# Kernel optimization log

Hardware: AMD Instinct MI355X
Metric: run time of the kernel (lower is better)

## Reference

```python
import jax, jax.numpy as jnp
import numpy as np

K = 16          # filter order (number of Laplacian powers)
MLP_OUT = 16    # mlp_hid == mlp_out for mlp_nlayers == 1
D_PE = 64       # phi output dim
BN_EPS = 1e-5
B, N, M = 8, 1024, 128
E = 131072


def setup_inputs() -> dict:
    key = jax.random.key(0)
    ks = jax.random.split(key, 12)
    # Symmetric, spectrally-bounded Laplacian surrogate so 15 matrix powers stay finite.
    A = jax.random.normal(ks[0], (B, N, N), dtype=jnp.float32)
    Lap = (A + jnp.swapaxes(A, -1, -2)) * (0.5 / jnp.sqrt(jnp.float32(N)))
    W = jax.random.normal(ks[1], (B, N, M), dtype=jnp.float32)
    edge_index = jax.random.randint(ks[2], (2, E), 0, B * N, dtype=jnp.int64)
    batch = jnp.repeat(jnp.arange(B, dtype=jnp.int64), N)
    # MLP layer (k -> MLP_OUT) + BatchNorm affine params
    lin_w = jax.random.normal(ks[3], (K, MLP_OUT), dtype=jnp.float32) / jnp.sqrt(jnp.float32(K))
    lin_b = jnp.zeros((MLP_OUT,), dtype=jnp.float32)
    bn_gamma = jnp.ones((MLP_OUT,), dtype=jnp.float32)
    bn_beta = jnp.zeros((MLP_OUT,), dtype=jnp.float32)
    # phi: GIN-style 2-layer MLP after neighbor aggregation
    phi_w1 = jax.random.normal(ks[4], (MLP_OUT, D_PE), dtype=jnp.float32) / jnp.sqrt(jnp.float32(MLP_OUT))
    phi_b1 = jnp.zeros((D_PE,), dtype=jnp.float32)
    phi_w2 = jax.random.normal(ks[5], (D_PE, D_PE), dtype=jnp.float32) / jnp.sqrt(jnp.float32(D_PE))
    phi_b2 = jnp.zeros((D_PE,), dtype=jnp.float32)
    return {"Lap": Lap, "W": W, "lin_w": lin_w, "lin_b": lin_b,
            "bn_gamma": bn_gamma, "bn_beta": bn_beta,
            "phi_w1": phi_w1, "phi_b1": phi_b1, "phi_w2": phi_w2, "phi_b2": phi_b2,
            "edge_index": edge_index, "batch": batch}


def _filter(S, W0):
    """Sequential power filter: returns [k, N, M] = [W0, S@W0, S^2@W0, ...]."""
    def step(out, _):
        nxt = S @ out
        return nxt, nxt
    _, rest = jax.lax.scan(step, W0, None, length=K - 1)
    return jnp.concatenate([W0[None], rest], axis=0)


def reference(Lap, W, lin_w, lin_b, bn_gamma, bn_beta,
              phi_w1, phi_b1, phi_w2, phi_b2, edge_index, batch):
    # Batched filter over all graphs: [B, k, N, M] -> [B, N, M, k]
    feat = jax.vmap(_filter)(Lap, W)
    feat = jnp.transpose(feat, (0, 2, 3, 1))
    # Linear over k -> MLP_OUT channels: [B, N, M, C]
    h = feat @ lin_w + lin_b
    # BatchNorm1d (training mode), per-graph statistics over (N, M) per channel,
    # matching the torch per-graph loop where BN sees [M, C, N].
    mean = jnp.mean(h, axis=(1, 2), keepdims=True)
    var = jnp.var(h, axis=(1, 2), keepdims=True)
    h = (h - mean) * jax.lax.rsqrt(var + BN_EPS) * bn_gamma + bn_beta
    h = jax.nn.relu(h)
    # phi: pool random-sample dim M, flatten graphs -> [N_sum, C]
    x = jnp.mean(h, axis=2).reshape(-1, h.shape[-1])
    src, dst = edge_index[0], edge_index[1]
    agg = jax.ops.segment_sum(x[src], dst, num_segments=x.shape[0])
    g = x + agg  # GIN aggregation
    out = jax.nn.relu(g @ phi_w1 + phi_b1) @ phi_w2 + phi_b2  # [N_sum, D_PE]
    return out
```

## Files before the change

### kernel.cpp

```cpp
#include <hip/hip_runtime.h>

#define B 8
#define N 1024
#define M 128
#define KF 16
#define C 16
#define DPE 64
#define NE 131072
#define NV (B*N)
#define NM (N*M)
#define BN_EPS 1e-5f

typedef short bf16x8 __attribute__((ext_vector_type(8)));
typedef float f32x4 __attribute__((ext_vector_type(4)));

__device__ inline unsigned short f2bf_rne(float f) {
    unsigned u = __float_as_uint(f);
    u += 0x7fffu + ((u >> 16) & 1u);
    return (unsigned short)(u >> 16);
}
__device__ inline float bf2f(unsigned short s) {
    return __uint_as_float((unsigned)s << 16);
}
__device__ inline void split_bf16(float v, unsigned short& hi, unsigned short& lo) {
    hi = f2bf_rne(v);
    float hf = __uint_as_float((unsigned)hi << 16);
    lo = f2bf_rne(v - hf);
}
union U4 { uint4 v; unsigned short s[8]; };
union U2 { uint2 v; unsigned short s[4]; };

__device__ __host__ inline size_t PF4(int b, int msub, int ks, int hl, int l) {
    return ((((size_t)b * 8 + msub) * 32 + ks) * 2 + hl) * 64 + l;
}
#define PFBUF ((size_t)B * 8 * 32 * 2 * 64)

__global__ __launch_bounds__(256) void prep_all(const float* __restrict__ W,
                                                const int* __restrict__ ei,
                                                uint4* __restrict__ Pf,
                                                unsigned short* __restrict__ feat,
                                                int* __restrict__ cnt) {
    __shared__ float T[32][33];
    int blk = blockIdx.x;
    int t = threadIdx.x;
    if (blk < 1024) {
        int r = blk;
        int b = r & 7;
        int tile = r >> 3;
        int nt = tile & 31, mt = tile >> 5;
        int n0 = nt * 32, m0 = mt * 32;
        {
            int nl = t >> 3, mq = t & 7;
            float4 v = *(const float4*)(W + ((size_t)b * N + n0 + nl) * M + m0 + mq * 4);
            T[nl][mq * 4 + 0] = v.x; T[nl][mq * 4 + 1] = v.y;
            T[nl][mq * 4 + 2] = v.z; T[nl][mq * 4 + 3] = v.w;
        }
        __syncthreads();
        {
            int ml = t >> 3, nq = t & 7;
            U2 o;
            o.s[0] = f2bf_rne(T[nq * 4 + 0][ml]);
            o.s[1] = f2bf_rne(T[nq * 4 + 1][ml]);
            o.s[2] = f2bf_rne(T[nq * 4 + 2][ml]);
            o.s[3] = f2bf_rne(T[nq * 4 + 3][ml]);
            unsigned short* plane = feat + (size_t)b * KF * NM;
            *(uint2*)(plane + (size_t)(m0 + ml) * N + n0 + nq * 4) = o.v;
        }
    } else if (blk < 1536) {
        int r0 = blk - 1024;
        int b = r0 & 7;
        int r = (r0 >> 3) * 256 + t;
        int msub = r >> 11, ks = (r >> 6) & 31, l = r & 63;
        int m = 16 * msub + (l & 15);
        U4 hi, lo;
        #pragma unroll
        for (int j = 0; j < 8; j++) {
            int n = 32 * ks + 8 * (l >> 4) + j;
            float v = W[((size_t)b * N + n) * M + m];
            split_bf16(v, hi.s[j], lo.s[j]);
        }
        Pf[PF4(b, msub, ks, 0, l)] = hi.v;
        Pf[PF4(b, msub, ks, 1, l)] = lo.v;
    } else {
        int e = (blk - 1536) * 256 + t;
        bool is64 = (ei[1] == 0 && ei[3] == 0 && ei[5] == 0 && ei[7] == 0);
        int dst = is64 ? ei[2 * (NE + e)] : ei[NE + e];
        atomicAdd(&cnt[dst], 1);
    }
}

__global__ __launch_bounds__(512) void gemm_chain(const float* __restrict__ Lap,
                                                  uint4* __restrict__ PfA,
                                                  uint4* __restrict__ PfB,
                                                  unsigned short* __restrict__ feat,
                                                  unsigned* bar) {
    extern __shared__ __align__(16) char smem[];
    uint4* ldsS = (uint4*)smem;
    float* Dl = (float*)(smem + 131072);

    int b = blockIdx.x & 7, bx = blockIdx.x >> 3;
    int t = threadIdx.x;
    int w = t >> 6, lane = t & 63;
    int wq = w >> 1, h = w & 1;
    int n0 = 32 * bx;

    {
        int nl = t >> 4;
        int kg = t & 15;
        const float* row = Lap + ((size_t)b * N + n0 + nl) * N;
        int base = (nl >> 4) * 4096;
        #pragma unroll
        for (int jj = 0; jj < 8; jj++) {
            int koct = kg + 16 * jj;
            int k0 = koct * 8;
            float4 f0 = *(const float4*)(row + k0);
            float4 f1 = *(const float4*)(row + k0 + 4);
            float e[8] = {f0.x, f0.y, f0.z, f0.w, f1.x, f1.y, f1.z, f1.w};
            U4 hi, lo;
            #pragma unroll
            for (int j = 0; j < 8; j++) split_bf16(e[j], hi.s[j], lo.s[j]);
            int ks = koct >> 2;
            int l = (nl & 15) + 16 * (koct & 3);
            ldsS[base + ks * 128 + l] = hi.v;
            ldsS[base + ks * 128 + 64 + l] = lo.v;
        }
    }
    __syncthreads();

    #pragma unroll 1
    for (int k = 0; k < KF - 1; k++) {
        const uint4* PfIn = (k & 1) ? PfB : PfA;
        uint4* PfOut      = (k & 1) ? PfA : PfB;
        const uint4* Pw0 = PfIn + (size_t)(b * 8 + 2 * wq) * 4096;
        const uint4* Pw1 = Pw0 + 4096;
        const uint4* ldsB = ldsS + h * 4096;

        f32x4 acc0 = {}, acc1 = {};
        uint4 ph[4][2], pl[4][2];
        #pragma unroll
        for (int q = 0; q < 4; q++) {
            ph[q][0] = Pw0[(size_t)q * 128 + lane];
            pl[q][0] = Pw0[(size_t)q * 128 + 64 + lane];
            ph[q][1] = Pw1[(size_t)q * 128 + lane];
            pl[q][1] = Pw1[(size_t)q * 128 + 64 + lane];
        }
        #pragma unroll
        for (int ks = 0; ks < 32; ks++) {
            int slot = ks & 3;
            uint4 a0h = ph[slot][0], a0l = pl[slot][0];
            uint4 a1h = ph[slot][1], a1l = pl[slot][1];
            if (ks < 28) {
                ph[slot][0] = Pw0[(size_t)(ks + 4) * 128 + lane];
                pl[slot][0] = Pw0[(size_t)(ks + 4) * 128 + 64 + lane];
                ph[slot][1] = Pw1[(size_t)(ks + 4) * 128 + lane];
                pl[slot][1] = Pw1[(size_t)(ks + 4) * 128 + 64 + lane];
            }
            bf16x8 bh = __builtin_bit_cast(bf16x8, ldsB[ks * 128 + lane]);
            bf16x8 bl = __builtin_bit_cast(bf16x8, ldsB[ks * 128 + 64 + lane]);
            bf16x8 A0h = __builtin_bit_cast(bf16x8, a0h);
            bf16x8 A0l = __builtin_bit_cast(bf16x8, a0l);
            bf16x8 A1h = __builtin_bit_cast(bf16x8, a1h);
            bf16x8 A1l = __builtin_bit_cast(bf16x8, a1l);
            acc0 = __builtin_amdgcn_mfma_f32_16x16x32_bf16(A0h, bh, acc0, 0, 0, 0);
            acc0 = __builtin_amdgcn_mfma_f32_16x16x32_bf16(A0h, bl, acc0, 0, 0, 0);
            acc0 = __builtin_amdgcn_mfma_f32_16x16x32_bf16(A0l, bh, acc0, 0, 0, 0);
            acc1 = __builtin_amdgcn_mfma_f32_16x16x32_bf16(A1h, bh, acc1, 0, 0, 0);
            acc1 = __builtin_amdgcn_mfma_f32_16x16x32_bf16(A1h, bl, acc1, 0, 0, 0);
            acc1 = __builtin_amdgcn_mfma_f32_16x16x32_bf16(A1l, bh, acc1, 0, 0, 0);
        }

        #pragma unroll
        for (int r = 0; r < 4; r++) {
            int m = 32 * wq + 4 * (lane >> 4) + r;
            Dl[m * 36 + 16 * h + (lane & 15)] = acc0[r];
            Dl[(m + 16) * 36 + 16 * h + (lane & 15)] = acc1[r];
        }
        __syncthreads();

        {
            int m = t >> 2, c0 = (t & 3) * 8;
            float4 v0 = *(const float4*)&Dl[m * 36 + c0];
            float4 v1 = *(const float4*)&Dl[m * 36 + c0 + 4];
            float e[8] = {v0.x, v0.y, v0.z, v0.w, v1.x, v1.y, v1.z, v1.w};
            U4 hi, lo;
            #pragma unroll
            for (int j = 0; j < 8; j++) split_bf16(e[j], hi.s[j], lo.s[j]);
            unsigned short* plane = feat + ((size_t)b * KF + (k + 1)) * NM
                                        + (size_t)m * N + n0 + c0;
            *(uint4*)plane = hi.v;
            if (k < KF - 2) {
                int l = (m & 15) + 16 * (c0 >> 3);
                PfOut[PF4(b, m >> 4, bx, 0, l)] = hi.v;
                PfOut[PF4(b, m >> 4, bx, 1, l)] = lo.v;
            }
        }
        if (k < KF - 2) {
            __syncthreads();
            if (t == 0) {
                __hip_atomic_fetch_add(&bar[b * 32], 1u, __ATOMIC_RELAXED,
                                       __HIP_MEMORY_SCOPE_AGENT);
                unsigned target = 32u * (unsigned)(k + 1);
                while (__hip_atomic_load(&bar[b * 32], __ATOMIC_RELAXED,
                                         __HIP_MEMORY_SCOPE_AGENT) < target)
                    __builtin_amdgcn_s_sleep(1);
            }
            __syncthreads();
            asm volatile("buffer_inv sc0\n\ts_waitcnt vmcnt(0)" ::: "memory");
        }
    }
}

__global__ __launch_bounds__(256) void bn_stats_scan(const unsigned short* __restrict__ feat,
                                                     const float* __restrict__ lin_w,
                                                     const float* __restrict__ lin_b,
                                                     float* __restrict__ stats,
                                                     const int* __restrict__ cnt,
                                                     int* __restrict__ off,
                                                     int* __restrict__ cur) {
    __shared__ float wls[KF * C];
    __shared__ float red[4][2][C];
    __shared__ int ss[256];
    int t = threadIdx.x;
    if (blockIdx.x < 8) {
        if (blockIdx.x == 0) {
            int base = t * 32;
            int local[32];
            int s = 0;
            #pragma unroll
            for (int i = 0; i < 32; i++) { local[i] = cnt[base + i]; s += local[i]; }
            ss[t] = s;
            __syncthreads();
            #pragma unroll
            for (int d = 1; d < 256; d <<= 1) {
                int v = (t >= d) ? ss[t - d] : 0;
                __syncthreads();
                ss[t] += v;
                __syncthreads();
            }
            int excl = ss[t] - s;
            #pragma unroll
            for (int i = 0; i < 32; i++) { off[base + i] = excl; cur[base + i] = excl; excl += local[i]; }
        }
        return;
    }
    int blk = blockIdx.x - 8;
    wls[t] = lin_w[t];
    __syncthreads();
    int b = blk & 7;
    int i = (blk >> 3) * 256 + t;
    const uint2* fb = (const uint2*)(feat + (size_t)b * KF * NM);

    float4 hacc[C];
    #pragma unroll
    for (int c = 0; c < C; c++) {
        float bb = lin_b[c];
        hacc[c] = make_float4(bb, bb, bb, bb);
    }
    for (int kk = 0; kk < KF; kk++) {
        U2 u; u.v = fb[(size_t)kk * (NM / 4) + i];
        float p0 = bf2f(u.s[0]), p1 = bf2f(u.s[1]), p2 = bf2f(u.s[2]), p3 = bf2f(u.s[3]);
        #pragma unroll
        for (int c = 0; c < C; c++) {
            float wv = wls[kk * C + c];
            hacc[c].x = fmaf(p0, wv, hacc[c].x);
            hacc[c].y = fmaf(p1, wv, hacc[c].y);
            hacc[c].z = fmaf(p2, wv, hacc[c].z);
            hacc[c].w = fmaf(p3, wv, hacc[c].w);
        }
    }
    float s[C], ssq[C];
    #pragma unroll
    for (int c = 0; c < C; c++) {
        float4 hh = hacc[c];
        s[c] = hh.x + hh.y + hh.z + hh.w;
        ssq[c] = hh.x * hh.x + hh.y * hh.y + hh.z * hh.z + hh.w * hh.w;
    }
    #pragma unroll
    for (int o = 32; o > 0; o >>= 1)
        #pragma unroll
        for (int c = 0; c < C; c++) {
            s[c] += __shfl_down(s[c], o);
            ssq[c] += __shfl_down(ssq[c], o);
        }
    if ((t & 63) == 0) {
        int wv = t >> 6;
        #pragma unroll
        for (int c = 0; c < C; c++) { red[wv][0][c] = s[c]; red[wv][1][c] = ssq[c]; }
    }
    __syncthreads();
    if (t < 32) {
        int which = t >> 4, c = t & 15;
        float v = red[0][which][c] + red[1][which][c] + red[2][which][c] + red[3][which][c];
        atomicAdd(&stats[b * 32 + which * 16 + c], v);
    }
}

__global__ __launch_bounds__(256) void bnx_fill(const unsigned short* __restrict__ feat,
                                                const float* __restrict__ lin_w,
                                                const float* __restrict__ lin_b,
                                                const float* __restrict__ gam,
                                                const float* __restrict__ bet,
                                                const float* __restrict__ stats,
                                                float* __restrict__ x,
                                                const int* __restrict__ ei,
                                                int* __restrict__ cur,
                                                int* __restrict__ bucket) {
    __shared__ float wls[KF * C];
    __shared__ float red[8][32 * 17];
    int t = threadIdx.x;
    if (blockIdx.x >= 256) {
        int e = (blockIdx.x - 256) * 256 + t;
        bool is64 = (ei[1] == 0 && ei[3] == 0 && ei[5] == 0 && ei[7] == 0);
        int src, dst;
        if (is64) { src = ei[2 * e]; dst = ei[2 * (NE + e)]; }
        else      { src = ei[e];     dst = ei[NE + e]; }
        int pos = atomicAdd(&cur[dst], 1);
        bucket[pos] = src;
        return;
    }
    wls[t] = lin_w[t];
    __syncthreads();
    int grp = blockIdx.x;
    int b = grp & 7, n0 = (grp >> 3) * 32;
    int nl = t & 31, mg = t >> 5;
    int n = n0 + nl;

    const float inv_nm = 1.0f / (float)NM;
    float sc[C], sh[C], bb[C];
    #pragma unroll
    for (int c = 0; c < C; c++) {
        float mean = stats[b * 32 + c] * inv_nm;
        float var = stats[b * 32 + 16 + c] * inv_nm - mean * mean;
        sc[c] = gam[c] * rsqrtf(var + BN_EPS);
        sh[c] = bet[c] - mean * sc[c];
        bb[c] = lin_b[c];
    }
    const unsigned short* fb = feat + (size_t)b * KF * NM + n;
    float y[C] = {};
    for (int m = mg * 16; m < mg * 16 + 16; m++) {
        float p[KF];
        #pragma unroll
        for (int kk = 0; kk < KF; kk++) p[kk] = bf2f(fb[(size_t)kk * NM + (size_t)m * N]);
        #pragma unroll
        for (int c = 0; c < C; c++) {
            float hh = bb[c];
            #pragma unroll
            for (int kk = 0; kk < KF; kk++) hh = fmaf(p[kk], wls[kk * C + c], hh);
            y[c] += fmaxf(fmaf(hh, sc[c], sh[c]), 0.0f);
        }
    }
    #pragma unroll
    for (int c = 0; c < C; c++) red[mg][nl * 17 + c] = y[c];
    __syncthreads();
    #pragma unroll
    for (int q = 0; q < 2; q++) {
        int slot = t + q * 256;
        int snl = slot >> 4, c = slot & 15;
        float v = 0.0f;
        #pragma unroll
        for (int m8 = 0; m8 < 8; m8++) v += red[m8][snl * 17 + c];
        v *= (1.0f / (float)M);
        x[((size_t)b * N + n0 + snl) * C + c] = v;
    }
}

__global__ __launch_bounds__(256) void phi_fused(const int* __restrict__ cnt,
                                                 const int* __restrict__ off,
                                                 const int* __restrict__ bucket,
                                                 const float* __restrict__ x,
                                                 const float* __restrict__ w1,
                                                 const float* __restrict__ b1,
                                                 const float* __restrict__ w2,
                                                 const float* __restrict__ b2,
                                                 float* __restrict__ out) {
    __shared__ float w1s[C * DPE];
    __shared__ float w2s[DPE * DPE];
    __shared__ float b2s[DPE];
    __shared__ float gsh[16][17];
    __shared__ float h1sh[16][DPE];
    int t = threadIdx.x;
    #pragma unroll
    for (int q = 0; q < 4; q++) w1s[t + q * 256] = w1[t + q * 256];
    #pragma unroll
    for (int q = 0; q < 16; q++) w2s[t + q * 256] = w2[t + q * 256];
    if (t < DPE) b2s[t] = b2[t];

    {
        int nl = t >> 4, c = t & 15;
        int n = blockIdx.x * 16 + nl;
        int o = off[n], d = cnt[n];
        float v = x[(size_t)n * C + c];
        int j = 0;
        for (; j + 4 <= d; j += 4) {
            int s0 = bucket[o + j], s1 = bucket[o + j + 1];
            int s2 = bucket[o + j + 2], s3 = bucket[o + j + 3];
            v += x[(size_t)s0 * C + c];
            v += x[(size_t)s1 * C + c];
            v += x[(size_t)s2 * C + c];
            v += x[(size_t)s3 * C + c];
        }
        for (; j < d; j++) v += x[(size_t)bucket[o + j] * C + c];
        gsh[nl][c] = v;
    }
    __syncthreads();
    #pragma unroll
    for (int q = 0; q < 4; q++) {
        int item = t + 256 * q;
        int node = item >> 6, j = item & 63;
        float h = b1[j];
        #pragma unroll
        for (int c = 0; c < C; c++) h = fmaf(gsh[node][c], w1s[c * DPE + j], h);
        h1sh[node][j] = fmaxf(h, 0.0f);
    }
    __syncthreads();
    #pragma unroll
    for (int q = 0; q < 4; q++) {
        int item = t + 256 * q;
        int node = item >> 6, d = item & 63;
        float o2 = b2s[d];
        #pragma unroll
        for (int j = 0; j < DPE; j++) o2 = fmaf(h1sh[node][j], w2s[j * DPE + d], o2);
        out[((size_t)blockIdx.x * 16 + node) * DPE + d] = o2;
    }
}

extern "C" void kernel_launch(void* const* d_in, const int* in_sizes, int n_in,
                              void* d_out, int out_size, void* d_ws, size_t ws_size,
                              hipStream_t stream) {
    const float* Lap   = (const float*)d_in[0];
    const float* W     = (const float*)d_in[1];
    const float* lin_w = (const float*)d_in[2];
    const float* lin_b = (const float*)d_in[3];
    const float* gam   = (const float*)d_in[4];
    const float* bet   = (const float*)d_in[5];
    const float* w1    = (const float*)d_in[6];
    const float* b1    = (const float*)d_in[7];
    const float* w2    = (const float*)d_in[8];
    const float* b2    = (const float*)d_in[9];
    const int*   ei    = (const int*)d_in[10];

    char* wsb = (char*)d_ws;
    unsigned short* feat = (unsigned short*)wsb;
    uint4* Pf    = (uint4*)(wsb + ((size_t)32 << 20));
    char* tail   = wsb + ((size_t)40 << 20);
    float* stats = (float*)tail;
    unsigned* bar = (unsigned*)(tail + 1024);
    int* cnt     = (int*)(tail + 8192);
    float* x     = (float*)(tail + 40960);
    int* off     = (int*)(x + (size_t)NV * C);
    int* cur     = off + NV;
    int* bucket  = cur + NV;
    float* out   = (float*)d_out;

    static bool attr_set = false;
    if (!attr_set) {
        hipFuncSetAttribute((const void*)gemm_chain,
                            hipFuncAttributeMaxDynamicSharedMemorySize, 149504);
        attr_set = true;
    }

    hipMemsetAsync(tail, 0, 40960, stream);
    prep_all<<<dim3(2048), 256, 0, stream>>>(W, ei, Pf, feat, cnt);
    gemm_chain<<<dim3(256), 512, 149504, stream>>>(Lap, Pf, Pf + PFBUF, feat, bar);
    bn_stats_scan<<<dim3(1032), 256, 0, stream>>>(feat, lin_w, lin_b, stats, cnt, off, cur);
    bnx_fill<<<dim3(768), 256, 0, stream>>>(feat, lin_w, lin_b, gam, bet, stats, x, ei, cur, bucket);
    phi_fused<<<dim3(NV / 16), 256, 0, stream>>>(cnt, off, bucket, x, w1, b1, w2, b2, out);
}
```

Before: 319.4 us.

## Split K dimension across wave groups with 2x2 register tiles and LDS reduction

Each wave now computes a 32x32 output tile (2x2 MFMA accumulators) over half of the K range instead of a 32x16 tile over the full K. The two wave groups' partial sums are combined through LDS with an extra barrier. This raises operand reuse per loaded fragment, halving the redundant global loads of the P matrix per block, at the cost of an extra sync and LDS read-modify-write, more accumulator registers, and a shallower prefetch depth.

```diff
diff --git a/kernel.cpp b/kernel.cpp
--- a/kernel.cpp
+++ b/kernel.cpp
@@ -101,7 +101,7 @@
     int b = blockIdx.x & 7, bx = blockIdx.x >> 3;
     int t = threadIdx.x;
     int w = t >> 6, lane = t & 63;
-    int wq = w >> 1, h = w & 1;
+    int g = w >> 2, wq = w & 3;
     int n0 = 32 * bx;
 
     {
@@ -131,49 +131,75 @@
     for (int k = 0; k < KF - 1; k++) {
         const uint4* PfIn = (k & 1) ? PfB : PfA;
         uint4* PfOut      = (k & 1) ? PfA : PfB;
-        const uint4* Pw0 = PfIn + (size_t)(b * 8 + 2 * wq) * 4096;
+        const uint4* Pw0 = PfIn + (size_t)(b * 8 + 2 * wq) * 4096 + (size_t)(16 * g) * 128;
         const uint4* Pw1 = Pw0 + 4096;
-        const uint4* ldsB = ldsS + h * 4096;
-
-        f32x4 acc0 = {}, acc1 = {};
-        uint4 ph[4][2], pl[4][2];
-        #pragma unroll
-        for (int q = 0; q < 4; q++) {
+
+        f32x4 acc[2][2] = {};
+        uint4 ph[2][2], pl[2][2];
+        #pragma unroll
+        for (int q = 0; q < 2; q++) {
             ph[q][0] = Pw0[(size_t)q * 128 + lane];
             pl[q][0] = Pw0[(size_t)q * 128 + 64 + lane];
             ph[q][1] = Pw1[(size_t)q * 128 + lane];
             pl[q][1] = Pw1[(size_t)q * 128 + 64 + lane];
         }
-        #pragma unroll
-        for (int ks = 0; ks < 32; ks++) {
-            int slot = ks & 3;
-            uint4 a0h = ph[slot][0], a0l = pl[slot][0];
-            uint4 a1h = ph[slot][1], a1l = pl[slot][1];
-            if (ks < 28) {
-                ph[slot][0] = Pw0[(size_t)(ks + 4) * 128 + lane];
-                pl[slot][0] = Pw0[(size_t)(ks + 4) * 128 + 64 + lane];
-                ph[slot][1] = Pw1[(size_t)(ks + 4) * 128 + lane];
-                pl[slot][1] = Pw1[(size_t)(ks + 4) * 128 + 64 + lane];
+        #pragma unroll 2
+        for (int ks = 0; ks < 16; ks++) {
+            int kg = 16 * g + ks;
+            uint4 a0h = ph[ks & 1][0], a0l = pl[ks & 1][0];
+            uint4 a1h = ph[ks & 1][1], a1l = pl[ks & 1][1];
+            if (ks < 14) {
+                ph[ks & 1][0] = Pw0[(size_t)(ks + 2) * 128 + lane];
+                pl[ks & 1][0] = Pw0[(size_t)(ks + 2) * 128 + 64 + lane];
+                ph[ks & 1][1] = Pw1[(size_t)(ks + 2) * 128 + lane];
+                pl[ks & 1][1] = Pw1[(size_t)(ks + 2) * 128 + 64 + lane];
             }
-            bf16x8 bh = __builtin_bit_cast(bf16x8, ldsB[ks * 128 + lane]);
-            bf16x8 bl = __builtin_bit_cast(bf16x8, ldsB[ks * 128 + 64 + lane]);
+            bf16x8 b0h = __builtin_bit_cast(bf16x8, ldsS[kg * 128 + lane]);
+            bf16x8 b0l = __builtin_bit_cast(bf16x8, ldsS[kg * 128 + 64 + lane]);
+            bf16x8 b1h = __builtin_bit_cast(bf16x8, ldsS[4096 + kg * 128 + lane]);
+            bf16x8 b1l = __builtin_bit_cast(bf16x8, ldsS[4096 + kg * 128 + 64 + lane]);
             bf16x8 A0h = __builtin_bit_cast(bf16x8, a0h);
             bf16x8 A0l = __builtin_bit_cast(bf16x8, a0l);
             bf16x8 A1h = __builtin_bit_cast(bf16x8, a1h);
             bf16x8 A1l = __builtin_bit_cast(bf16x8, a1l);
-            acc0 = __builtin_amdgcn_mfma_f32_16x16x32_bf16(A0h, bh, acc0, 0, 0, 0);
-            acc0 = __builtin_amdgcn_mfma_f32_16x16x32_bf16(A0h, bl, acc0, 0, 0, 0);
-            acc0 = __builtin_amdgcn_mfma_f32_16x16x32_bf16(A0l, bh, acc0, 0, 0, 0);
-            acc1 = __builtin_amdgcn_mfma_f32_16x16x32_bf16(A1h, bh, acc1, 0, 0, 0);
-            acc1 = __builtin_amdgcn_mfma_f32_16x16x32_bf16(A1h, bl, acc1, 0, 0, 0);
-            acc1 = __builtin_amdgcn_mfma_f32_16x16x32_bf16(A1l, bh, acc1, 0, 0, 0);
-        }
-
-        #pragma unroll
-        for (int r = 0; r < 4; r++) {
-            int m = 32 * wq + 4 * (lane >> 4) + r;
-            Dl[m * 36 + 16 * h + (lane & 15)] = acc0[r];
-            Dl[(m + 16) * 36 + 16 * h + (lane & 15)] = acc1[r];
+            acc[0][0] = __builtin_amdgcn_mfma_f32_16x16x32_bf16(A0h, b0h, acc[0][0], 0, 0, 0);
+            acc[0][0] = __builtin_amdgcn_mfma_f32_16x16x32_bf16(A0h, b0l, acc[0][0], 0, 0, 0);
+            acc[0][0] = __builtin_amdgcn_mfma_f32_16x16x32_bf16(A0l, b0h, acc[0][0], 0, 0, 0);
+            acc[0][1] = __builtin_amdgcn_mfma_f32_16x16x32_bf16(A0h, b1h, acc[0][1], 0, 0, 0);
+            acc[0][1] = __builtin_amdgcn_mfma_f32_16x16x32_bf16(A0h, b1l, acc[0][1], 0, 0, 0);
+            acc[0][1] = __builtin_amdgcn_mfma_f32_16x16x32_bf16(A0l, b1h, acc[0][1], 0, 0, 0);
+            acc[1][0] = __builtin_amdgcn_mfma_f32_16x16x32_bf16(A1h, b0h, acc[1][0], 0, 0, 0);
+            acc[1][0] = __builtin_amdgcn_mfma_f32_16x16x32_bf16(A1h, b0l, acc[1][0], 0, 0, 0);
+            acc[1][0] = __builtin_amdgcn_mfma_f32_16x16x32_bf16(A1l, b0h, acc[1][0], 0, 0, 0);
+            acc[1][1] = __builtin_amdgcn_mfma_f32_16x16x32_bf16(A1h, b1h, acc[1][1], 0, 0, 0);
+            acc[1][1] = __builtin_amdgcn_mfma_f32_16x16x32_bf16(A1h, b1l, acc[1][1], 0, 0, 0);
+            acc[1][1] = __builtin_amdgcn_mfma_f32_16x16x32_bf16(A1l, b1h, acc[1][1], 0, 0, 0);
+        }
+
+        if (g == 1) {
+            #pragma unroll
+            for (int mi = 0; mi < 2; mi++)
+                #pragma unroll
+                for (int ni = 0; ni < 2; ni++)
+                    #pragma unroll
+                    for (int r = 0; r < 4; r++) {
+                        int m = 32 * wq + 16 * mi + 4 * (lane >> 4) + r;
+                        int c = 16 * ni + (lane & 15);
+                        Dl[m * 36 + c] = acc[mi][ni][r];
+                    }
+        }
+        __syncthreads();
+        if (g == 0) {
+            #pragma unroll
+            for (int mi = 0; mi < 2; mi++)
+                #pragma unroll
+                for (int ni = 0; ni < 2; ni++)
+                    #pragma unroll
+                    for (int r = 0; r < 4; r++) {
+                        int m = 32 * wq + 16 * mi + 4 * (lane >> 4) + r;
+                        int c = 16 * ni + (lane & 15);
+                        Dl[m * 36 + c] += acc[mi][ni][r];
+                    }
         }
         __syncthreads();
 
```

Result: faster. 275.9 us (-13.6%).
